# Performance work log

Measured on AMD Instinct MI355X. Metric: run time of the kernel, lower is better.

## Reference

```python
import jax, jax.numpy as jnp
import numpy as np

HIDDEN = 768
HEADS = 12
HEAD_DIM = HIDDEN // HEADS


def setup_inputs() -> dict:
    key = jax.random.key(0)
    ks = jax.random.split(key, 5)
    B, S = 1, 4096
    scale = 1.0 / np.sqrt(HIDDEN)
    return {
        "x": jax.random.normal(ks[0], (B, S, HIDDEN), dtype=jnp.float32),
        "w_qkv": jax.random.normal(ks[1], (HIDDEN, 3 * HIDDEN), dtype=jnp.float32) * scale,
        "b_qkv": jnp.zeros((3 * HIDDEN,), dtype=jnp.float32),
        "w_proj": jax.random.normal(ks[2], (HIDDEN, HIDDEN), dtype=jnp.float32) * scale,
        "b_proj": jnp.zeros((HIDDEN,), dtype=jnp.float32),
    }


def reference(x, w_qkv, b_qkv, w_proj, b_proj):
    B, S, D = x.shape
    H, Hd = HEADS, HEAD_DIM
    qkv = x @ w_qkv + b_qkv                        # [B,S,3D]
    qkv = qkv.reshape(B, S, 3, H, Hd)
    q, k, v = (jnp.moveaxis(qkv[:, :, i], 2, 1) for i in range(3))  # [B,H,S,Hd]
    scale = 1.0 / np.sqrt(Hd)
    attn = jnp.einsum("bhqd,bhkd->bhqk", q, k) * scale
    attn = jax.nn.softmax(attn, axis=-1)
    o = jnp.einsum("bhqk,bhkd->bhqd", attn, v)     # [B,H,S,Hd]
    o = jnp.moveaxis(o, 1, 2).reshape(B, S, D)
    return o @ w_proj + b_proj
```

## Files before the change

kernel.cpp:

```cpp
#include <hip/hip_runtime.h>

#define S_LEN 4096
#define DMODEL 768
#define NHEAD 12
#define HDIM 64
#define DQKV 2304

typedef __attribute__((ext_vector_type(8))) __bf16 bf16x8;
typedef __attribute__((ext_vector_type(4))) float f32x4;
typedef __attribute__((ext_vector_type(8))) unsigned short ushort8;

#define LOG2E 1.4426950408889634f

#if __has_builtin(__builtin_amdgcn_exp2f)
#define EXP2(x) __builtin_amdgcn_exp2f(x)
#else
#define EXP2(x) exp2f(x)
#endif

static __device__ __forceinline__ unsigned short f2bf(float f) {
  unsigned int u = __float_as_uint(f);
  u += 0x7FFFu + ((u >> 16) & 1u);
  return (unsigned short)(u >> 16);
}

static __device__ __forceinline__ void gload_lds16(const unsigned short* g, unsigned short* l) {
  __builtin_amdgcn_global_load_lds(
      (const __attribute__((address_space(1))) unsigned int*)g,
      (__attribute__((address_space(3))) unsigned int*)l, 16, 0, 0);
}

__global__ __launch_bounds__(256) void k_prep(const float* __restrict__ x,
                                              const float* __restrict__ w_qkv,
                                              const float* __restrict__ w_proj,
                                              unsigned short* __restrict__ xb,
                                              unsigned short* __restrict__ wqkvT,
                                              unsigned short* __restrict__ wprojT) {
  __shared__ unsigned short t[64 * 65];
  int bid = blockIdx.x;
  int tid = threadIdx.x;
  if (bid < 1536) {
    int i = (bid * 256 + tid) * 8;
    const float4* p = reinterpret_cast<const float4*>(x + i);
    float4 a = p[0], b = p[1];
    ushort8 r;
    r[0] = f2bf(a.x); r[1] = f2bf(a.y); r[2] = f2bf(a.z); r[3] = f2bf(a.w);
    r[4] = f2bf(b.x); r[5] = f2bf(b.y); r[6] = f2bf(b.z); r[7] = f2bf(b.w);
    *reinterpret_cast<ushort8*>(xb + i) = r;
    return;
  }
  const float* in;
  unsigned short* out;
  int Kdim, Ndim, bx, by;
  if (bid < 1968) {
    int tt = bid - 1536;
    in = w_qkv; out = wqkvT; Kdim = DMODEL; Ndim = DQKV;
    bx = tt % 36; by = tt / 36;
  } else {
    int tt = bid - 1968;
    in = w_proj; out = wprojT; Kdim = DMODEL; Ndim = DMODEL;
    bx = tt % 12; by = tt / 12;
  }
  int k0 = by * 64, n0 = bx * 64;
#pragma unroll
  for (int p = 0; p < 4; ++p) {
    int r = p * 16 + (tid >> 4);
    int c = (tid & 15) * 4;
    float4 v = *reinterpret_cast<const float4*>(in + (size_t)(k0 + r) * Ndim + n0 + c);
    t[(c + 0) * 65 + r] = f2bf(v.x);
    t[(c + 1) * 65 + r] = f2bf(v.y);
    t[(c + 2) * 65 + r] = f2bf(v.z);
    t[(c + 3) * 65 + r] = f2bf(v.w);
  }
  __syncthreads();
#pragma unroll
  for (int p = 0; p < 2; ++p) {
    int task = p * 256 + tid;
    int rr = task >> 3;
    int cc = (task & 7) * 8;
    ushort8 r;
#pragma unroll
    for (int j = 0; j < 8; ++j) r[j] = t[rr * 65 + cc + j];
    *reinterpret_cast<ushort8*>(out + (size_t)(n0 + rr) * Kdim + k0 + cc) = r;
  }
}

__global__ __launch_bounds__(256) void k_gemm_qkv(const unsigned short* __restrict__ A,
                                                  const unsigned short* __restrict__ Bt,
                                                  const float* __restrict__ bias,
                                                  unsigned short* __restrict__ Qb,
                                                  unsigned short* __restrict__ Kf,
                                                  unsigned short* __restrict__ Vf) {
  __shared__ unsigned short As[2][128 * 32];
  __shared__ unsigned short Bs[2][128 * 32];

  int tid = threadIdx.x;
  int lane = tid & 63, wave = tid >> 6;
  int wr = wave >> 1, wc = wave & 1;
  int m0 = blockIdx.y * 128, n0 = blockIdx.x * 128;
  int r16 = lane & 15, g = lane >> 4;

  int ca0 = wave * 2, ca1 = wave * 2 + 1;
  int srow = lane >> 2, scol = (lane & 3) * 8;

  f32x4 acc[4][4] = {};

#define GSTAGE(BUF, K0)                                                                 \
  do {                                                                                  \
    gload_lds16(A + (size_t)(m0 + ca0 * 16 + srow) * DMODEL + (K0) + scol,              \
                &As[BUF][ca0 * 512]);                                                   \
    gload_lds16(A + (size_t)(m0 + ca1 * 16 + srow) * DMODEL + (K0) + scol,              \
                &As[BUF][ca1 * 512]);                                                   \
    gload_lds16(Bt + (size_t)(n0 + ca0 * 16 + srow) * DMODEL + (K0) + scol,             \
                &Bs[BUF][ca0 * 512]);                                                   \
    gload_lds16(Bt + (size_t)(n0 + ca1 * 16 + srow) * DMODEL + (K0) + scol,             \
                &Bs[BUF][ca1 * 512]);                                                   \
  } while (0)

  GSTAGE(0, 0);
  for (int kt = 0; kt < DMODEL / 32; ++kt) {
    int cur = kt & 1;
    __syncthreads();

    bf16x8 af[4], bfr[4];
#pragma unroll
    for (int m = 0; m < 4; ++m)
      af[m] = *reinterpret_cast<const bf16x8*>(&As[cur][(wr * 64 + m * 16 + r16) * 32 + g * 8]);
#pragma unroll
    for (int n = 0; n < 4; ++n)
      bfr[n] = *reinterpret_cast<const bf16x8*>(&Bs[cur][(wc * 64 + n * 16 + r16) * 32 + g * 8]);

    if (kt < DMODEL / 32 - 1) GSTAGE(cur ^ 1, (kt + 1) * 32);

#pragma unroll
    for (int m = 0; m < 4; ++m)
#pragma unroll
      for (int n = 0; n < 4; ++n)
        acc[m][n] = __builtin_amdgcn_mfma_f32_16x16x32_bf16(af[m], bfr[n], acc[m][n], 0, 0, 0);
  }
#undef GSTAGE

#pragma unroll
  for (int m = 0; m < 4; ++m) {
    int grow0 = m0 + wr * 64 + m * 16 + 4 * g;
#pragma unroll
    for (int n = 0; n < 4; ++n) {
      int gcol = n0 + wc * 64 + n * 16 + r16;
      float bv = bias[gcol];
      int sect = gcol / DMODEL;
      int rem = gcol - sect * DMODEL;
      int h = rem >> 6, hd = rem & 63;
      if (sect == 2) {
        int j = hd >> 4, r16v = hd & 15;
        int tile = grow0 >> 6, kk = (grow0 >> 5) & 1, g2 = (grow0 >> 3) & 3, e0 = grow0 & 7;
        size_t base = (((size_t)h * 64 + tile) * 8 + (j * 2 + kk)) * 512 +
                      (size_t)(g2 * 16 + r16v) * 8 + e0;
        ushort4 pk;
        pk.x = f2bf(acc[m][n][0] + bv);
        pk.y = f2bf(acc[m][n][1] + bv);
        pk.z = f2bf(acc[m][n][2] + bv);
        pk.w = f2bf(acc[m][n][3] + bv);
        *reinterpret_cast<ushort4*>(Vf + base) = pk;
      } else if (sect == 0) {
#pragma unroll
        for (int i = 0; i < 4; ++i)
          Qb[((size_t)h * S_LEN + grow0 + i) * HDIM + hd] =
              f2bf((acc[m][n][i] + bv) * (0.125f * LOG2E));
      } else {
        int kk = hd >> 5, g2 = (hd >> 3) & 3, e = hd & 7;
#pragma unroll
        for (int i = 0; i < 4; ++i) {
          int s = grow0 + i;
          int tile = s >> 6, r = s & 63;
          int j = (((r >> 2) & 1) << 1) | (r >> 5);
          int r16l = (r & 3) | (((r >> 3) & 3) << 2);
          size_t idx = (((size_t)h * 64 + tile) * 8 + (j * 2 + kk)) * 512 +
                       (size_t)(g2 * 16 + r16l) * 8 + e;
          Kf[idx] = f2bf(acc[m][n][i] + bv);
        }
      }
    }
  }
}

__global__ __launch_bounds__(256) void k_gemm_proj(const unsigned short* __restrict__ A,
                                                   const unsigned short* __restrict__ Bt,
                                                   const float* __restrict__ bias,
                                                   float* __restrict__ outf) {
  __shared__ unsigned short As[2][64 * 32];
  __shared__ unsigned short Bs[2][64 * 32];

  int tid = threadIdx.x;
  int lane = tid & 63, wave = tid >> 6;
  int wr = wave >> 1, wc = wave & 1;
  int m0 = blockIdx.y * 64, n0 = blockIdx.x * 64;
  int r16 = lane & 15, g = lane >> 4;
  int srow = lane >> 2, scol = (lane & 3) * 8;

  f32x4 acc[2][2] = {};

#define GSTAGE(BUF, K0)                                                                 \
  do {                                                                                  \
    gload_lds16(A + (size_t)(m0 + wave * 16 + srow) * DMODEL + (K0) + scol,             \
                &As[BUF][wave * 512]);                                                  \
    gload_lds16(Bt + (size_t)(n0 + wave * 16 + srow) * DMODEL + (K0) + scol,            \
                &Bs[BUF][wave * 512]);                                                  \
  } while (0)

  GSTAGE(0, 0);
  for (int kt = 0; kt < DMODEL / 32; ++kt) {
    int cur = kt & 1;
    __syncthreads();

    bf16x8 af[2], bfr[2];
#pragma unroll
    for (int m = 0; m < 2; ++m)
      af[m] = *reinterpret_cast<const bf16x8*>(&As[cur][(wr * 32 + m * 16 + r16) * 32 + g * 8]);
#pragma unroll
    for (int n = 0; n < 2; ++n)
      bfr[n] = *reinterpret_cast<const bf16x8*>(&Bs[cur][(wc * 32 + n * 16 + r16) * 32 + g * 8]);

    if (kt < DMODEL / 32 - 1) GSTAGE(cur ^ 1, (kt + 1) * 32);

#pragma unroll
    for (int m = 0; m < 2; ++m)
#pragma unroll
      for (int n = 0; n < 2; ++n)
        acc[m][n] = __builtin_amdgcn_mfma_f32_16x16x32_bf16(af[m], bfr[n], acc[m][n], 0, 0, 0);
  }
#undef GSTAGE

#pragma unroll
  for (int m = 0; m < 2; ++m) {
    int grow0 = m0 + wr * 32 + m * 16 + 4 * g;
#pragma unroll
    for (int n = 0; n < 2; ++n) {
      int gcol = n0 + wc * 32 + n * 16 + r16;
      float bv = bias[gcol];
#pragma unroll
      for (int i = 0; i < 4; ++i)
        outf[(size_t)(grow0 + i) * DMODEL + gcol] = acc[m][n][i] + bv;
    }
  }
}

__global__ __launch_bounds__(256, 3) void k_attn(const unsigned short* __restrict__ Q,
                                                 const unsigned short* __restrict__ Kf,
                                                 const unsigned short* __restrict__ Vf,
                                                 float* __restrict__ Opart,
                                                 float* __restrict__ Lpart,
                                                 float* __restrict__ Mpart) {
  __shared__ unsigned short ldsK[2][4096];
  __shared__ unsigned short ldsV[2][4096];

  int tid = threadIdx.x;
  int lane = tid & 63, wave = tid >> 6;
  int r16 = lane & 15, g = lane >> 4;

  int bid = blockIdx.x;
  int gid = (bid & 7) * 192 + (bid >> 3);
  int h = gid >> 7;
  int rem = gid & 127;
  int quarter = rem & 3;
  int qb = rem >> 2;
  int qbaseA = qb * 128 + wave * 16;
  int qbaseB = qbaseA + 64;
  int tb = quarter * 16;

  const unsigned short* KfH = Kf + (size_t)h * (64 * 4096);
  const unsigned short* VfH = Vf + (size_t)h * (64 * 4096);
  float* OpH = Opart + ((size_t)quarter * NHEAD + h) * S_LEN * HDIM;
  float* LpH = Lpart + ((size_t)quarter * NHEAD + h) * S_LEN;
  float* MpH = Mpart + ((size_t)quarter * NHEAD + h) * S_LEN;

  const unsigned short* qpA = Q + ((size_t)h * S_LEN + qbaseA + r16) * HDIM + g * 8;
  const unsigned short* qpB = Q + ((size_t)h * S_LEN + qbaseB + r16) * HDIM + g * 8;
  bf16x8 qf0a = *reinterpret_cast<const bf16x8*>(qpA);
  bf16x8 qf1a = *reinterpret_cast<const bf16x8*>(qpA + 32);
  bf16x8 qf0b = *reinterpret_cast<const bf16x8*>(qpB);
  bf16x8 qf1b = *reinterpret_cast<const bf16x8*>(qpB + 32);

  f32x4 oaccA[4] = {}, oaccB[4] = {};
  f32x4 lsumA = {}, lsumB = {};
  f32x4 zinitA = {}, zinitB = {};
  float mrowA = 0.f, mrowB = 0.f;
  bf16x8 bones;
#pragma unroll
  for (int e = 0; e < 8; ++e) bones[e] = (__bf16)1.0f;

  int c0 = wave, c1 = wave + 4;

#define STAGE(BUF, T)                                                        \
  do {                                                                       \
    const unsigned short* kg_ = KfH + (size_t)(T) * 4096;                    \
    const unsigned short* vg_ = VfH + (size_t)(T) * 4096;                    \
    gload_lds16(kg_ + c0 * 512 + lane * 8, &ldsK[BUF][c0 * 512]);            \
    gload_lds16(kg_ + c1 * 512 + lane * 8, &ldsK[BUF][c1 * 512]);            \
    gload_lds16(vg_ + c0 * 512 + lane * 8, &ldsV[BUF][c0 * 512]);            \
    gload_lds16(vg_ + c1 * 512 + lane * 8, &ldsV[BUF][c1 * 512]);            \
  } while (0)

#define QK(SARR, QF0, QF1, ZI)                                                          \
  do {                                                                                  \
    _Pragma("unroll") for (int j_ = 0; j_ < 4; ++j_) {                                  \
      f32x4 z_ = ZI;                                                                    \
      z_ = __builtin_amdgcn_mfma_f32_16x16x32_bf16(kfr_[2 * j_], QF0, z_, 0, 0, 0);     \
      SARR[j_] = __builtin_amdgcn_mfma_f32_16x16x32_bf16(kfr_[2 * j_ + 1], QF1, z_, 0, 0, 0); \
    }                                                                                   \
  } while (0)

#define SOFTPV(SARR, MROW, ZI, LSUM, OACC, FIRST)                                       \
  do {                                                                                  \
    float x1_ = fmaxf(fmaxf(SARR[0][0], SARR[0][1]), SARR[0][2]);                       \
    float x2_ = fmaxf(fmaxf(SARR[0][3], SARR[1][0]), SARR[1][1]);                       \
    float x3_ = fmaxf(fmaxf(SARR[1][2], SARR[1][3]), SARR[2][0]);                       \
    float x4_ = fmaxf(fmaxf(SARR[2][1], SARR[2][2]), SARR[2][3]);                       \
    float x5_ = fmaxf(fmaxf(SARR[3][0], SARR[3][1]), SARR[3][2]);                       \
    float pm_ = fmaxf(fmaxf(fmaxf(x1_, x2_), fmaxf(x3_, x4_)), fmaxf(x5_, SARR[3][3])); \
    pm_ = fmaxf(pm_, __shfl_xor(pm_, 16));                                              \
    pm_ = fmaxf(pm_, __shfl_xor(pm_, 32));                                              \
    if (FIRST) {                                                                        \
      _Pragma("unroll") for (int j_ = 0; j_ < 4; ++j_)                                  \
        _Pragma("unroll") for (int i_ = 0; i_ < 4; ++i_) SARR[j_][i_] -= pm_;           \
      MROW = pm_;                                                                       \
      ZI[0] = -MROW; ZI[1] = -MROW; ZI[2] = -MROW; ZI[3] = -MROW;                       \
    } else if (__any(pm_ > 8.f)) {                                                      \
      float dl_ = fmaxf(pm_, 0.f);                                                      \
      float al_ = EXP2(-dl_);                                                           \
      float a0_ = __shfl(al_, 20 * g + 0), a1_ = __shfl(al_, 20 * g + 1);               \
      float a2_ = __shfl(al_, 20 * g + 2), a3_ = __shfl(al_, 20 * g + 3);               \
      LSUM[0] *= a0_; LSUM[1] *= a1_; LSUM[2] *= a2_; LSUM[3] *= a3_;                   \
      _Pragma("unroll") for (int j_ = 0; j_ < 4; ++j_) {                                \
        OACC[j_][0] *= a0_; OACC[j_][1] *= a1_;                                         \
        OACC[j_][2] *= a2_; OACC[j_][3] *= a3_;                                         \
      }                                                                                 \
      _Pragma("unroll") for (int j_ = 0; j_ < 4; ++j_)                                  \
        _Pragma("unroll") for (int i_ = 0; i_ < 4; ++i_) SARR[j_][i_] -= dl_;           \
      MROW += dl_;                                                                      \
      ZI[0] = -MROW; ZI[1] = -MROW; ZI[2] = -MROW; ZI[3] = -MROW;                       \
    }                                                                                   \
    float p_[4][4];                                                                     \
    _Pragma("unroll") for (int j_ = 0; j_ < 4; ++j_)                                    \
      _Pragma("unroll") for (int i_ = 0; i_ < 4; ++i_)                                  \
        p_[j_][i_] = EXP2(SARR[j_][i_]);                                                \
    bf16x8 pa0_, pa1_;                                                                  \
    _Pragma("unroll") for (int e_ = 0; e_ < 8; ++e_) {                                  \
      pa0_[e_] = (__bf16)p_[2 * (e_ >> 2)][e_ & 3];                                     \
      pa1_[e_] = (__bf16)p_[1 + 2 * (e_ >> 2)][e_ & 3];                                 \
    }                                                                                   \
    LSUM = __builtin_amdgcn_mfma_f32_16x16x32_bf16(pa0_, bones, LSUM, 0, 0, 0);         \
    LSUM = __builtin_amdgcn_mfma_f32_16x16x32_bf16(pa1_, bones, LSUM, 0, 0, 0);         \
    _Pragma("unroll") for (int j_ = 0; j_ < 4; ++j_) {                                  \
      OACC[j_] = __builtin_amdgcn_mfma_f32_16x16x32_bf16(pa0_, vfr_[2 * j_], OACC[j_], 0, 0, 0); \
      OACC[j_] = __builtin_amdgcn_mfma_f32_16x16x32_bf16(pa1_, vfr_[2 * j_ + 1], OACC[j_], 0, 0, 0); \
    }                                                                                   \
  } while (0)

#define BODY(CUR, DO_STAGE, T, FIRSTF)                                                  \
  do {                                                                                  \
    __syncthreads();                                                                    \
    bf16x8 kfr_[8], vfr_[8];                                                            \
    _Pragma("unroll") for (int f_ = 0; f_ < 8; ++f_) {                                  \
      kfr_[f_] = *reinterpret_cast<const bf16x8*>(&ldsK[CUR][f_ * 512 + lane * 8]);     \
      vfr_[f_] = *reinterpret_cast<const bf16x8*>(&ldsV[CUR][f_ * 512 + lane * 8]);     \
    }                                                                                   \
    if (DO_STAGE) STAGE((CUR) ^ 1, (T) + 1);                                            \
    f32x4 sA_[4], sB_[4];                                                               \
    QK(sA_, qf0a, qf1a, zinitA);                                                        \
    QK(sB_, qf0b, qf1b, zinitB);                                                        \
    SOFTPV(sA_, mrowA, zinitA, lsumA, oaccA, FIRSTF);                                   \
    SOFTPV(sB_, mrowB, zinitB, lsumB, oaccB, FIRSTF);                                   \
  } while (0)

  STAGE(0, tb);
  BODY(0, true, tb, true);
  for (int pr = 0; pr < 7; ++pr) {
    BODY(1, true, tb + 2 * pr + 1, false);
    BODY(0, true, tb + 2 * pr + 2, false);
  }
  BODY(1, false, tb + 15, false);
#undef BODY
#undef SOFTPV
#undef QK
#undef STAGE

#pragma unroll
  for (int i = 0; i < 4; ++i) {
    int srowA = qbaseA + 4 * g + i;
    int srowB = qbaseB + 4 * g + i;
#pragma unroll
    for (int j = 0; j < 4; ++j) {
      int col = j * 16 + r16;
      OpH[(size_t)srowA * HDIM + col] = oaccA[j][i];
      OpH[(size_t)srowB * HDIM + col] = oaccB[j][i];
    }
  }
  if (g == 0) {
    MpH[qbaseA + r16] = mrowA;
    MpH[qbaseB + r16] = mrowB;
  }
  if (r16 == 0) {
#pragma unroll
    for (int i = 0; i < 4; ++i) {
      LpH[qbaseA + 4 * g + i] = lsumA[i];
      LpH[qbaseB + 4 * g + i] = lsumB[i];
    }
  }
}

__global__ __launch_bounds__(256) void k_combine(const float* __restrict__ Opart,
                                                 const float* __restrict__ Lpart,
                                                 const float* __restrict__ Mpart,
                                                 unsigned short* __restrict__ O) {
  int gidx = blockIdx.x * 256 + threadIdx.x;
  int h = gidx >> 15;
  int rem = gidx & 32767;
  int s = rem >> 3;
  int d0 = (rem & 7) * 8;
  size_t i0 = (size_t)h * S_LEN + s;
  size_t o0 = i0 * HDIM + d0;
  const size_t HS_O = (size_t)NHEAD * S_LEN * HDIM;
  const size_t HS_L = (size_t)NHEAD * S_LEN;

  float m0 = Mpart[i0], m1 = Mpart[HS_L + i0];
  float m2 = Mpart[2 * HS_L + i0], m3 = Mpart[3 * HS_L + i0];
  float l0 = Lpart[i0], l1 = Lpart[HS_L + i0];
  float l2 = Lpart[2 * HS_L + i0], l3 = Lpart[3 * HS_L + i0];
  float m = fmaxf(fmaxf(m0, m1), fmaxf(m2, m3));
  float w0 = EXP2(m0 - m), w1 = EXP2(m1 - m), w2 = EXP2(m2 - m), w3 = EXP2(m3 - m);
  float inv = 1.0f / (l0 * w0 + l1 * w1 + l2 * w2 + l3 * w3);

  float acc[8];
#pragma unroll
  for (int q = 0; q < 4; ++q) {
    float w = (q == 0) ? w0 : (q == 1) ? w1 : (q == 2) ? w2 : w3;
    const float* src = Opart + q * HS_O + o0;
    float4 a = *reinterpret_cast<const float4*>(src);
    float4 b = *reinterpret_cast<const float4*>(src + 4);
    if (q == 0) {
      acc[0] = a.x * w; acc[1] = a.y * w; acc[2] = a.z * w; acc[3] = a.w * w;
      acc[4] = b.x * w; acc[5] = b.y * w; acc[6] = b.z * w; acc[7] = b.w * w;
    } else {
      acc[0] += a.x * w; acc[1] += a.y * w; acc[2] += a.z * w; acc[3] += a.w * w;
      acc[4] += b.x * w; acc[5] += b.y * w; acc[6] += b.z * w; acc[7] += b.w * w;
    }
  }
  ushort8 r;
#pragma unroll
  for (int e = 0; e < 8; ++e) r[e] = f2bf(acc[e] * inv);
  *reinterpret_cast<ushort8*>(O + (size_t)s * DMODEL + h * HDIM + d0) = r;
}

extern "C" void kernel_launch(void* const* d_in, const int* in_sizes, int n_in,
                              void* d_out, int out_size, void* d_ws, size_t ws_size,
                              hipStream_t stream) {
  const float* x = (const float*)d_in[0];
  const float* w_qkv = (const float*)d_in[1];
  const float* b_qkv = (const float*)d_in[2];
  const float* w_proj = (const float*)d_in[3];
  const float* b_proj = (const float*)d_in[4];
  float* out = (float*)d_out;

  unsigned short* ws16 = (unsigned short*)d_ws;
  unsigned short* xb = ws16;
  unsigned short* wqkvT = xb + (size_t)S_LEN * DMODEL;
  unsigned short* wprojT = wqkvT + (size_t)DQKV * DMODEL;
  unsigned short* Qb = wprojT + (size_t)DMODEL * DMODEL;
  unsigned short* Kf = Qb + (size_t)NHEAD * S_LEN * HDIM;
  unsigned short* Vf = Kf + (size_t)NHEAD * S_LEN * HDIM;
  float* Opart = (float*)(Vf + (size_t)NHEAD * S_LEN * HDIM);
  float* Lpart = Opart + (size_t)4 * NHEAD * S_LEN * HDIM;
  float* Mpart = Lpart + (size_t)4 * NHEAD * S_LEN;
  unsigned short* Ob = xb;

  k_prep<<<2112, 256, 0, stream>>>(x, w_qkv, w_proj, xb, wqkvT, wprojT);
  k_gemm_qkv<<<dim3(DQKV / 128, S_LEN / 128), 256, 0, stream>>>(xb, wqkvT, b_qkv, Qb, Kf, Vf);
  k_attn<<<1536, 256, 0, stream>>>(Qb, Kf, Vf, Opart, Lpart, Mpart);
  k_combine<<<(NHEAD * S_LEN * 8) / 256, 256, 0, stream>>>(Opart, Lpart, Mpart, Ob);
  k_gemm_proj<<<dim3(DMODEL / 64, S_LEN / 64), 256, 0, stream>>>(Ob, wprojT, b_proj, out);
}
```

Before: 126.6 us.

## Split attention KV into halves instead of quarters and raise MFMA wave priority

The attention kernel now splits each head's key/value sequence into two halves rather than four. The grid shrinks to 768 blocks, each looping over 32 KV tiles, and the partial O/L/M buffers and the combine kernel shrink to two partials. This cuts partial-result write and read traffic and the combine work, at the cost of fewer blocks on the GPU and longer per-block loops. It also wraps the MFMA sections in s_setprio so waves issuing matrix ops get scheduling priority over waves doing softmax.

```diff
diff --git a/kernel.cpp b/kernel.cpp
--- a/kernel.cpp
+++ b/kernel.cpp
@@ -258,20 +258,20 @@
   int r16 = lane & 15, g = lane >> 4;
 
   int bid = blockIdx.x;
-  int gid = (bid & 7) * 192 + (bid >> 3);
-  int h = gid >> 7;
-  int rem = gid & 127;
-  int quarter = rem & 3;
-  int qb = rem >> 2;
+  int gid = (bid & 7) * 96 + (bid >> 3);
+  int h = gid >> 6;
+  int rem = gid & 63;
+  int half = rem & 1;
+  int qb = rem >> 1;
   int qbaseA = qb * 128 + wave * 16;
   int qbaseB = qbaseA + 64;
-  int tb = quarter * 16;
+  int tb = half * 32;
 
   const unsigned short* KfH = Kf + (size_t)h * (64 * 4096);
   const unsigned short* VfH = Vf + (size_t)h * (64 * 4096);
-  float* OpH = Opart + ((size_t)quarter * NHEAD + h) * S_LEN * HDIM;
-  float* LpH = Lpart + ((size_t)quarter * NHEAD + h) * S_LEN;
-  float* MpH = Mpart + ((size_t)quarter * NHEAD + h) * S_LEN;
+  float* OpH = Opart + ((size_t)half * NHEAD + h) * S_LEN * HDIM;
+  float* LpH = Lpart + ((size_t)half * NHEAD + h) * S_LEN;
+  float* MpH = Mpart + ((size_t)half * NHEAD + h) * S_LEN;
 
   const unsigned short* qpA = Q + ((size_t)h * S_LEN + qbaseA + r16) * HDIM + g * 8;
   const unsigned short* qpB = Q + ((size_t)h * S_LEN + qbaseB + r16) * HDIM + g * 8;
@@ -302,11 +302,13 @@
 
 #define QK(SARR, QF0, QF1, ZI)                                                          \
   do {                                                                                  \
+    __builtin_amdgcn_s_setprio(1);                                                      \
     _Pragma("unroll") for (int j_ = 0; j_ < 4; ++j_) {                                  \
       f32x4 z_ = ZI;                                                                    \
       z_ = __builtin_amdgcn_mfma_f32_16x16x32_bf16(kfr_[2 * j_], QF0, z_, 0, 0, 0);     \
       SARR[j_] = __builtin_amdgcn_mfma_f32_16x16x32_bf16(kfr_[2 * j_ + 1], QF1, z_, 0, 0, 0); \
     }                                                                                   \
+    __builtin_amdgcn_s_setprio(0);                                                      \
   } while (0)
 
 #define SOFTPV(SARR, MROW, ZI, LSUM, OACC, FIRST)                                       \
@@ -348,12 +350,14 @@
       pa0_[e_] = (__bf16)p_[2 * (e_ >> 2)][e_ & 3];                                     \
       pa1_[e_] = (__bf16)p_[1 + 2 * (e_ >> 2)][e_ & 3];                                 \
     }                                                                                   \
+    __builtin_amdgcn_s_setprio(1);                                                      \
     LSUM = __builtin_amdgcn_mfma_f32_16x16x32_bf16(pa0_, bones, LSUM, 0, 0, 0);         \
     LSUM = __builtin_amdgcn_mfma_f32_16x16x32_bf16(pa1_, bones, LSUM, 0, 0, 0);         \
     _Pragma("unroll") for (int j_ = 0; j_ < 4; ++j_) {                                  \
       OACC[j_] = __builtin_amdgcn_mfma_f32_16x16x32_bf16(pa0_, vfr_[2 * j_], OACC[j_], 0, 0, 0); \
       OACC[j_] = __builtin_amdgcn_mfma_f32_16x16x32_bf16(pa1_, vfr_[2 * j_ + 1], OACC[j_], 0, 0, 0); \
     }                                                                                   \
+    __builtin_amdgcn_s_setprio(0);                                                      \
   } while (0)
 
 #define BODY(CUR, DO_STAGE, T, FIRSTF)                                                  \
@@ -374,11 +378,11 @@
 
   STAGE(0, tb);
   BODY(0, true, tb, true);
-  for (int pr = 0; pr < 7; ++pr) {
+  for (int pr = 0; pr < 15; ++pr) {
     BODY(1, true, tb + 2 * pr + 1, false);
     BODY(0, true, tb + 2 * pr + 2, false);
   }
-  BODY(1, false, tb + 15, false);
+  BODY(1, false, tb + 31, false);
 #undef BODY
 #undef SOFTPV
 #undef QK
@@ -423,31 +427,23 @@
   const size_t HS_L = (size_t)NHEAD * S_LEN;
 
   float m0 = Mpart[i0], m1 = Mpart[HS_L + i0];
-  float m2 = Mpart[2 * HS_L + i0], m3 = Mpart[3 * HS_L + i0];
   float l0 = Lpart[i0], l1 = Lpart[HS_L + i0];
-  float l2 = Lpart[2 * HS_L + i0], l3 = Lpart[3 * HS_L + i0];
-  float m = fmaxf(fmaxf(m0, m1), fmaxf(m2, m3));
-  float w0 = EXP2(m0 - m), w1 = EXP2(m1 - m), w2 = EXP2(m2 - m), w3 = EXP2(m3 - m);
-  float inv = 1.0f / (l0 * w0 + l1 * w1 + l2 * w2 + l3 * w3);
-
-  float acc[8];
-#pragma unroll
-  for (int q = 0; q < 4; ++q) {
-    float w = (q == 0) ? w0 : (q == 1) ? w1 : (q == 2) ? w2 : w3;
-    const float* src = Opart + q * HS_O + o0;
-    float4 a = *reinterpret_cast<const float4*>(src);
-    float4 b = *reinterpret_cast<const float4*>(src + 4);
-    if (q == 0) {
-      acc[0] = a.x * w; acc[1] = a.y * w; acc[2] = a.z * w; acc[3] = a.w * w;
-      acc[4] = b.x * w; acc[5] = b.y * w; acc[6] = b.z * w; acc[7] = b.w * w;
-    } else {
-      acc[0] += a.x * w; acc[1] += a.y * w; acc[2] += a.z * w; acc[3] += a.w * w;
-      acc[4] += b.x * w; acc[5] += b.y * w; acc[6] += b.z * w; acc[7] += b.w * w;
-    }
-  }
+  float m = fmaxf(m0, m1);
+  float w0 = EXP2(m0 - m), w1 = EXP2(m1 - m);
+  float inv = 1.0f / (l0 * w0 + l1 * w1);
+  float4 a0 = *reinterpret_cast<const float4*>(Opart + o0);
+  float4 a1 = *reinterpret_cast<const float4*>(Opart + o0 + 4);
+  float4 b0 = *reinterpret_cast<const float4*>(Opart + HS_O + o0);
+  float4 b1 = *reinterpret_cast<const float4*>(Opart + HS_O + o0 + 4);
   ushort8 r;
-#pragma unroll
-  for (int e = 0; e < 8; ++e) r[e] = f2bf(acc[e] * inv);
+  r[0] = f2bf((a0.x * w0 + b0.x * w1) * inv);
+  r[1] = f2bf((a0.y * w0 + b0.y * w1) * inv);
+  r[2] = f2bf((a0.z * w0 + b0.z * w1) * inv);
+  r[3] = f2bf((a0.w * w0 + b0.w * w1) * inv);
+  r[4] = f2bf((a1.x * w0 + b1.x * w1) * inv);
+  r[5] = f2bf((a1.y * w0 + b1.y * w1) * inv);
+  r[6] = f2bf((a1.z * w0 + b1.z * w1) * inv);
+  r[7] = f2bf((a1.w * w0 + b1.w * w1) * inv);
   *reinterpret_cast<ushort8*>(O + (size_t)s * DMODEL + h * HDIM + d0) = r;
 }
 
@@ -469,13 +465,13 @@
   unsigned short* Kf = Qb + (size_t)NHEAD * S_LEN * HDIM;
   unsigned short* Vf = Kf + (size_t)NHEAD * S_LEN * HDIM;
   float* Opart = (float*)(Vf + (size_t)NHEAD * S_LEN * HDIM);
-  float* Lpart = Opart + (size_t)4 * NHEAD * S_LEN * HDIM;
-  float* Mpart = Lpart + (size_t)4 * NHEAD * S_LEN;
+  float* Lpart = Opart + (size_t)2 * NHEAD * S_LEN * HDIM;
+  float* Mpart = Lpart + (size_t)2 * NHEAD * S_LEN;
   unsigned short* Ob = xb;
 
   k_prep<<<2112, 256, 0, stream>>>(x, w_qkv, w_proj, xb, wqkvT, wprojT);
   k_gemm_qkv<<<dim3(DQKV / 128, S_LEN / 128), 256, 0, stream>>>(xb, wqkvT, b_qkv, Qb, Kf, Vf);
-  k_attn<<<1536, 256, 0, stream>>>(Qb, Kf, Vf, Opart, Lpart, Mpart);
+  k_attn<<<768, 256, 0, stream>>>(Qb, Kf, Vf, Opart, Lpart, Mpart);
   k_combine<<<(NHEAD * S_LEN * 8) / 256, 256, 0, stream>>>(Opart, Lpart, Mpart, Ob);
   k_gemm_proj<<<dim3(DMODEL / 64, S_LEN / 64), 256, 0, stream>>>(Ob, wprojT, b_proj, out);
 }
```

Result: slower. 142.5 us (+12.6%).
